# Kernel tuning notes

Hardware: AMD Instinct MI355X
Metric: run time of the kernel (lower is better)

## Reference

```python
import jax, jax.numpy as jnp
import numpy as np

B, N, DIM, HID, H, K, NNEG, MAXLEN, NUMALL = 4096, 50, 64, 64, 4, 10, 4, 512, 100000
NITEM = 50  # config onesample_size


def pe_table(max_len, dim):
    pos = jnp.arange(max_len, dtype=jnp.float32)[:, None]
    div = jnp.exp(jnp.arange(0, dim, 2, dtype=jnp.float32) * (-np.log(10000.0) / dim))
    ang = pos * div
    pe = jnp.zeros((max_len, dim), jnp.float32)
    return pe.at[:, 0::2].set(jnp.sin(ang)).at[:, 1::2].set(jnp.cos(ang))


def gat(x, adj, W_gat, a_src, a_dst, W_o):
    # x: (b,n,d), adj: (b,n,n) binary
    Wh = jnp.einsum('bnd,hdk->bhnk', x, W_gat)
    es = jnp.einsum('bhnk,hk->bhn', Wh, a_src)
    ed = jnp.einsum('bhnk,hk->bhn', Wh, a_dst)
    e = jax.nn.leaky_relu(es[:, :, :, None] + ed[:, :, None, :], 0.2)
    e = jnp.where(adj[:, None] > 0, e, -1e9)
    attn = jax.nn.softmax(e, axis=-1)
    out = jnp.einsum('bhnm,bhmk->bhnk', attn, Wh)
    out = out.transpose(0, 2, 1, 3).reshape(x.shape[0], x.shape[1], -1)
    return jax.nn.elu(out @ W_o)


def aggregate(x, cand):
    # attention-pool x (b,n,d) per candidate (b,c,d) -> (b,c,d)
    attn = jax.nn.softmax(jnp.einsum('bnd,bcd->bcn', x, cand), axis=-1)
    return jnp.einsum('bcn,bnd->bcd', attn, x)


def ssl_topk(user, pos, neg, tao=0.5):
    nrm = lambda v: v / jnp.linalg.norm(v, axis=-1, keepdims=True)
    user, pos, neg = nrm(user), nrm(pos), nrm(neg)
    ps = jnp.sum(jnp.exp(jnp.einsum('bkd,bd->bk', pos, user) / tao), axis=1)
    ns = jnp.sum(jnp.exp(jnp.einsum('bkd,bd->bk', neg, user) / tao), axis=1)
    return -jnp.mean(jnp.log(ps) - jnp.log(ps + ns))


def setup_inputs():
    key = jax.random.key(0)
    ks = jax.random.split(key, 14)
    d = {}
    d['emb_table'] = jax.random.normal(ks[0], (NUMALL + 1, DIM)) * 0.1
    d['W_PE'] = jax.random.normal(ks[1], (DIM, DIM)) * 0.1
    d['W_pred'] = jax.random.normal(ks[2], (2 * DIM, DIM)) * 0.1
    d['W_gat'] = jax.random.normal(ks[3], (H, DIM, HID)) * 0.1
    d['a_src'] = jax.random.normal(ks[4], (H, HID)) * 0.1
    d['a_dst'] = jax.random.normal(ks[5], (H, HID)) * 0.1
    d['W_o'] = jax.random.normal(ks[6], (H * HID, DIM)) * 0.1
    d['W_assign'] = jax.random.normal(ks[7], (DIM, K)) * 0.1
    d['adj'] = (jax.random.uniform(ks[8], (B, N, N)) > 0.5).astype(jnp.float32)
    d['history'] = jax.random.randint(ks[9], (B, N), 0, NUMALL)
    d['timestp'] = jax.random.randint(ks[10], (B, N), 0, MAXLEN)
    d['pos_id'] = jax.random.randint(ks[11], (B, 1), 0, NUMALL)
    d['neg_id'] = jax.random.randint(ks[12], (B, NNEG), 0, NUMALL)
    d['stp'] = jax.random.randint(ks[13], (B, 1), 0, MAXLEN)
    return d


def reference(emb_table, W_PE, W_pred, W_gat, a_src, a_dst, W_o, W_assign,
              adj, history, timestp, pos_id, neg_id, stp):
    pe = pe_table(MAXLEN, DIM)
    _x = emb_table[history]            # (B,N,D)
    pos = emb_table[pos_id]            # (B,1,D)
    neg = emb_table[neg_id]            # (B,NNEG,D)
    cand = jnp.concatenate([pos, neg], axis=1)  # (B,C,D)
    mask_base = (history > 0)[:, :, None].astype(_x.dtype)
    x = (_x + pe[timestp] @ W_PE) * mask_base
    cand = cand + pe[stp] @ W_PE       # broadcast PE over all candidates
    # ParentNodeLayer: soft assignment pooling (DiffPool-style)
    s = jax.nn.softmax(x @ W_assign, axis=-1)          # (B,N,K)
    x_parent = jnp.einsum('bnk,bnd->bkd', s, x)        # (B,K,D)
    # GAT over item sub-graph
    x_new_I = gat(x[:, :NITEM], adj[:, :NITEM, :NITEM], W_gat, a_src, a_dst, W_o)
    # candidate-conditioned aggregation + prediction (vectorized over candidates)
    u_F = aggregate(x_parent, cand)
    u_I = aggregate(x_new_I, cand)
    u = jnp.concatenate([u_F, u_I], axis=-1) @ W_pred  # (B,C,D)
    scores = jnp.sum(u * cand, axis=-1)                # (B,C)
    pos_s, neg_s = scores[:, :1], scores[:, 1:]
    loss = jnp.mean(jax.nn.softplus(neg_s - pos_s))
    s_m = s[:, :NITEM]
    loss_entropy = -jnp.sum(s_m * jnp.log(s_m)) / (NITEM * B)
    loss_reg = (jnp.sum(_x ** 2) + jnp.sum(pos ** 2) + jnp.sum(neg ** 2)) / float(B) \
               + jnp.sum(W_pred ** 2) + jnp.sum(W_PE ** 2)
    # contrastive branch (dropout in eval mode == identity)
    user_I = jnp.mean(x_new_I, axis=1)
    user_F = jnp.mean(x_parent, axis=1)
    sI = jnp.einsum('bcd,bd->bc', cand, user_I)
    sF = jnp.einsum('bcd,bd->bc', cand, user_F)
    n_cand = cand.shape[1]
    _, ind_I = jax.lax.top_k(sI, n_cand)
    _, ind_F = jax.lax.top_k(sF, n_cand)
    gather = lambda ind: jnp.take_along_axis(cand, ind[:, :, None], axis=1)
    C = 2
    loss_con = ssl_topk(user_I, gather(ind_F[:, :2]), gather(ind_F[:, 2:2 + C])) \
             + ssl_topk(user_F, gather(ind_I[:, :2]), gather(ind_I[:, 2:2 + C]))
    return jnp.stack([loss, loss_reg, loss_entropy, loss_con])
```

## Files before the change

kernel.cpp:

```cpp
#include <hip/hip_runtime.h>
#include <hip/hip_bf16.h>
#include <math.h>

typedef __hip_bfloat16 bf16;
typedef __attribute__((ext_vector_type(8))) short sv8;
typedef __attribute__((ext_vector_type(4))) short sv4;
typedef __attribute__((ext_vector_type(4))) float fv4;

__device__ __forceinline__ float b2f(bf16 v){ return __bfloat162float(v); }
__device__ __forceinline__ bf16  f2b(float v){ return __float2bfloat16(v); }
__device__ __forceinline__ short f2bs(float v){ bf16 h=__float2bfloat16(v); short s; __builtin_memcpy(&s,&h,2); return s; }
__device__ __forceinline__ float bs2f(short s){ bf16 h; __builtin_memcpy(&h,&s,2); return __bfloat162float(h); }
__device__ __forceinline__ fv4 MFMA(sv8 a, sv8 b, fv4 c){
  return __builtin_amdgcn_mfma_f32_16x16x32_bf16(a,b,c,0,0,0);
}
__device__ __forceinline__ int pk2(float a, float b){
  unsigned sa=(unsigned short)f2bs(a);
  unsigned sb=((unsigned)(unsigned short)f2bs(b))<<16;
  return (int)(sa|sb);
}
__device__ __forceinline__ int pk2s(short a, short b){
  return (int)(((unsigned short)a) | (((unsigned)(unsigned short)b)<<16));
}
union U8 { int i[4]; sv8 v; };

__global__ __launch_bounds__(64) void k_pe(const float* __restrict__ Wpe, float* __restrict__ pewt)
{
  const int t=blockIdx.x, d=threadIdx.x;
  __shared__ float pr[64];
  const float c0 = -logf(10000.f)/32.f;
  float ang = (float)t * expf((float)(d>>1)*c0);
  pr[d] = (d&1)? cosf(ang) : sinf(ang);
  __syncthreads();
  float a=0.f;
  #pragma unroll 8
  for(int j=0;j<64;j++) a += pr[j]*Wpe[j*64+d];
  pewt[t*64+d]=a;
}

__global__ __launch_bounds__(256) void k_prep(
    const float* __restrict__ Wg, const float* __restrict__ Wo,
    const float* __restrict__ as_, const float* __restrict__ ad_,
    const float* __restrict__ Wassign, const float* __restrict__ Wpred,
    short* __restrict__ wgb, short* __restrict__ wob, short* __restrict__ asb,
    short* __restrict__ wab, short* __restrict__ wpb)
{
  int i = blockIdx.x*256+threadIdx.x;
  {
    int j=i&7, lane=(i>>3)&63, ks=(i>>9)&1, nt=(i>>10)&3, h=(i>>12)&3;
    int c=lane&15, q=lane>>4;
    int k=ks*32+q*8+j;
    wgb[i] = f2bs(Wg[h*4096 + k*64 + nt*16 + c]);
    wob[i] = f2bs(Wo[(size_t)(h*64 + k)*64 + nt*16 + c]);
  }
  if(i<4096){
    int j=i&7, lane=(i>>3)&63, ks=(i>>9)&1, h=(i>>10)&3;
    int c=lane&15, q=lane>>4; int k=ks*32+q*8+j;
    float v = (c==0)? as_[h*64+k] : (c==1? ad_[h*64+k] : 0.f);
    asb[i]=f2bs(v);
  }
  if(i<1024){
    int j=i&7, lane=(i>>3)&63, ks=(i>>9)&1;
    int c=lane&15, q=lane>>4; int k=ks*32+q*8+j;
    wab[i] = (c<10)? f2bs(Wassign[k*10+c]) : (short)0;
  }
  if(i<8192){
    int j=i&7, lane=(i>>3)&63, ks=(i>>9)&3, nt=(i>>11)&3;
    int c=lane&15, q=lane>>4; int k=ks*32+q*8+j;
    wpb[i] = f2bs(Wpred[k*64 + nt*16 + c]);
  }
}

__global__ __launch_bounds__(256,4) void kmain(
    const float* __restrict__ emb, const float* __restrict__ pewt,
    const int* __restrict__ history, const int* __restrict__ timestp,
    const int* __restrict__ pos_id, const int* __restrict__ neg_id, const int* __restrict__ stp,
    const float* __restrict__ adj,
    const short* __restrict__ wgb, const short* __restrict__ wob, const short* __restrict__ asb,
    const short* __restrict__ wab, const short* __restrict__ wpb,
    float* __restrict__ reg_part, float* __restrict__ ent_part,
    float* __restrict__ loss_part, float* __restrict__ con_part)
{
  const int b=blockIdx.x, tid=threadIdx.x;
  const int h=tid>>6, lane=tid&63;
  const int c=lane&15, q=lane>>4;

  __shared__ __align__(16) char arena[36864];
  char*  PP    = arena + h*7200;
  short* xs_s  = (short*)(arena+14400);
  float* es_f  = (float*)(arena+28800 + h*768);
  float* ed_f  = es_f + 64;
  float* inv_f = es_f + 128;
  float* cndF  = (float*)(arena+31872);
  float* xplF  = (float*)(arena+33152);
  float* uFvec = (float*)(arena+35712);
  float* uacc  = (float*)(arena+35968);
  int*   hist  = (int*)(arena+36224);
  int*   tvals = (int*)(arena+36424);
  int*   ids   = (int*)(arena+36624);
  int*   stv   = (int*)(arena+36644);
  float* ph    = (float*)(arena+36648);
  float* scF   = (float*)(arena+36664);
  float* sIv   = scF+5;
  float* sFv   = scF+10;
  float* cnv   = scF+15;
  float* un    = scF+20;
  float* sbF   = (float*)arena;

  if (tid < 50) hist[tid] = history[b*50+tid];
  if (tid >= 64 && tid < 114) tvals[tid-64] = timestp[b*50+(tid-64)];
  if (tid == 128) stv[0] = stp[b];
  if (tid == 129) ids[0] = pos_id[b];
  if (tid >= 130 && tid < 134) ids[tid-129] = neg_id[b*4+(tid-130)];

  unsigned long long mymask=0ULL;
  {
    const float* adjb = adj + (size_t)b*2500;
    for(int n=0;n<50;n++){
      float av = (lane<50)? adjb[n*50+lane] : 0.f;
      unsigned long long mk = __ballot(av>0.f);
      if(lane==n) mymask = mk;
    }
  }
  __syncthreads();

  float regp=0.f;
  for (int i=tid;i<3200;i+=256){
    int n=i>>6, d=i&63;
    float ev=emb[(size_t)hist[n]*64 + d];
    regp += ev*ev;
    float v = (hist[n]>0) ? (ev + pewt[tvals[n]*64+d]) : 0.f;
    xs_s[n*72+d]=f2bs(v);
  }
  for (int i=tid;i<320;i+=256){
    int cc=i>>6, d=i&63;
    float ev=emb[(size_t)ids[cc]*64+d];
    regp += ev*ev;
    cndF[i]=ev + pewt[stv[0]*64+d];
  }
  #pragma unroll
  for(int m=1;m<64;m<<=1) regp += __shfl_xor(regp,m,64);
  if(lane==0) ph[h]=regp;
  __syncthreads();

  sv8 af[4][2];
  #pragma unroll
  for(int mt=0;mt<4;mt++){
    int r = mt*16 + c; if(r>=50) r=0;
    #pragma unroll
    for(int ks=0;ks<2;ks++)
      af[mt][ks] = *(const sv8*)(xs_s + r*72 + ks*32 + q*8);
  }
  {
    sv8 wa0 = *(const sv8*)(wab + (0*64+lane)*8);
    sv8 wa1 = *(const sv8*)(wab + (1*64+lane)*8);
    fv4 acc={0.f,0.f,0.f,0.f};
    acc = MFMA(af[h][0], wa0, acc);
    acc = MFMA(af[h][1], wa1, acc);
    #pragma unroll
    for(int reg=0;reg<4;reg++){
      int n=16*h+4*q+reg;
      if(n<50 && c<10) sbF[n*10+c]=acc[reg];
    }
  }
  __syncthreads();
  if(tid==0) reg_part[b]=ph[0]+ph[1]+ph[2]+ph[3];

  float entp=0.f;
  if (tid<50){
    float mx=-1e30f;
    for(int k=0;k<10;k++) mx=fmaxf(mx, sbF[tid*10+k]);
    float e[10], sm=0.f;
    for(int k=0;k<10;k++){ e[k]=expf(sbF[tid*10+k]-mx); sm+=e[k]; }
    float inv=1.f/sm;
    for(int k=0;k<10;k++){ float sv=e[k]*inv; sbF[tid*10+k]=sv; entp += sv*logf(sv); }
  }
  if(h==0){
    #pragma unroll
    for(int m=1;m<64;m<<=1) entp += __shfl_xor(entp,m,64);
    if(lane==0) ent_part[b]=entp;
  }
  __syncthreads();

  {
    sv8 sa[2], sxb[2];
    #pragma unroll
    for(int ks=0;ks<2;ks++){
      U8 ua, ub_;
      #pragma unroll
      for(int t2=0;t2<4;t2++){
        int n0=32*ks+8*q+2*t2, n1=n0+1;
        short lo=(n0<50 && c<10)? f2bs(sbF[n0*10+c]) : (short)0;
        short hi=(n1<50 && c<10)? f2bs(sbF[n1*10+c]) : (short)0;
        ua.i[t2]=pk2s(lo,hi);
        short lo2=(n0<50)? xs_s[n0*72+16*h+c] : (short)0;
        short hi2=(n1<50)? xs_s[n1*72+16*h+c] : (short)0;
        ub_.i[t2]=pk2s(lo2,hi2);
      }
      sa[ks]=ua.v; sxb[ks]=ub_.v;
    }
    fv4 acc={0.f,0.f,0.f,0.f};
    acc = MFMA(sa[0], sxb[0], acc);
    acc = MFMA(sa[1], sxb[1], acc);
    #pragma unroll
    for(int reg=0;reg<4;reg++){
      int k=4*q+reg;
      if(k<10) xplF[k*64+16*h+c]=acc[reg];
    }
  }
  __syncthreads();
  if(tid<64){
    float a=0.f;
    for(int k=0;k<10;k++) a += xplF[(k<<6)+tid];
    uFvec[tid]=a*0.1f;
  }

  int wh_pk[4][4][2];
  #pragma unroll
  for(int nt=0;nt<4;nt++){
    sv8 b0 = *(const sv8*)(wgb + (((h*4+nt)*2+0)*64 + lane)*8);
    sv8 b1 = *(const sv8*)(wgb + (((h*4+nt)*2+1)*64 + lane)*8);
    #pragma unroll
    for(int mt=0;mt<4;mt++){
      fv4 acc={0.f,0.f,0.f,0.f};
      acc = MFMA(af[mt][0], b0, acc);
      acc = MFMA(af[mt][1], b1, acc);
      wh_pk[mt][nt][0]=pk2(acc[0],acc[1]);
      wh_pk[mt][nt][1]=pk2(acc[2],acc[3]);
    }
  }
  {
    sv8 a5b0 = *(const sv8*)(asb + ((h*2+0)*64 + lane)*8);
    sv8 a5b1 = *(const sv8*)(asb + ((h*2+1)*64 + lane)*8);
    #pragma unroll
    for(int mt=0;mt<4;mt++){
      fv4 acc={0.f,0.f,0.f,0.f};
      acc = MFMA(af[mt][0], a5b0, acc);
      acc = MFMA(af[mt][1], a5b1, acc);
      if(c==0){
        #pragma unroll
        for(int reg=0;reg<4;reg++) es_f[mt*16+4*q+reg]=acc[reg];
      } else if(c==1){
        #pragma unroll
        for(int reg=0;reg<4;reg++) ed_f[mt*16+4*q+reg]=acc[reg];
      }
    }
  }
  {
    float es_n = es_f[lane];
    float sum=0.f;
    #pragma unroll
    for(int mb=0;mb<48;mb+=4){
      sv4 wv;
      #pragma unroll
      for(int jj=0;jj<4;jj++){
        int m=mb+jj;
        float z = es_n + ed_f[m];
        float lr = (z>0.f)? z : 0.2f*z;
        float p = ((mymask>>m)&1ULL)? expf(lr) : 0.f;
        wv[jj]=f2bs(p); sum+=p;
      }
      if(lane<50) *(sv4*)(PP + lane*144 + mb*2) = wv;
    }
    {
      sv4 wv={0,0,0,0};
      #pragma unroll
      for(int jj=0;jj<2;jj++){
        int m=48+jj;
        float z = es_n + ed_f[m];
        float lr = (z>0.f)? z : 0.2f*z;
        float p = ((mymask>>m)&1ULL)? expf(lr) : 0.f;
        wv[jj]=f2bs(p); sum+=p;
      }
      if(lane<50){
        *(sv4*)(PP + lane*144 + 48*2) = wv;
        sv4 zz={0,0,0,0};
        *(sv4*)(PP + lane*144 + 52*2) = zz;
        *(sv4*)(PP + lane*144 + 56*2) = zz;
        *(sv4*)(PP + lane*144 + 60*2) = zz;
      }
    }
    inv_f[lane] = (lane<50)? 1.f/sum : 0.f;
  }
  {
    sv8 ap[4][2];
    #pragma unroll
    for(int mt=0;mt<4;mt++){
      int r = mt*16+c; if(r>=50) r=0;
      #pragma unroll
      for(int ks=0;ks<2;ks++)
        ap[mt][ks] = *(const sv8*)(PP + r*144 + (ks*32+q*8)*2);
    }
    float invr[16];
    #pragma unroll
    for(int mt=0;mt<4;mt++)
      #pragma unroll
      for(int reg=0;reg<4;reg++) invr[mt*4+reg]=inv_f[mt*16+4*q+reg];

    const int L = c + ((q&1)<<5);
    const bool hi = (q>>1)!=0;
    #pragma unroll
    for(int nt=0;nt<4;nt++){
      sv8 bfr[2];
      #pragma unroll
      for(int ks=0;ks<2;ks++){
        int a0=__shfl(wh_pk[2*ks+0][nt][0],L,64), b0=__shfl(wh_pk[2*ks+1][nt][0],L,64);
        int a1=__shfl(wh_pk[2*ks+0][nt][1],L,64), b1=__shfl(wh_pk[2*ks+1][nt][1],L,64);
        int a2=__shfl(wh_pk[2*ks+0][nt][0],L+16,64), b2=__shfl(wh_pk[2*ks+1][nt][0],L+16,64);
        int a3=__shfl(wh_pk[2*ks+0][nt][1],L+16,64), b3=__shfl(wh_pk[2*ks+1][nt][1],L+16,64);
        U8 u;
        u.i[0]=hi?b0:a0; u.i[1]=hi?b1:a1; u.i[2]=hi?b2:a2; u.i[3]=hi?b3:a3;
        bfr[ks]=u.v;
      }
      #pragma unroll
      for(int mt=0;mt<4;mt++){
        fv4 acc={0.f,0.f,0.f,0.f};
        acc = MFMA(ap[mt][0], bfr[0], acc);
        acc = MFMA(ap[mt][1], bfr[1], acc);
        #pragma unroll
        for(int reg=0;reg<4;reg++){
          int row=mt*16+4*q+reg;
          if(row<50)
            *(short*)(PP + row*144 + (nt*16+c)*2) = f2bs(acc[reg]*invr[mt*4+reg]);
        }
      }
    }
  }
  {
    sv8 ao[4][2];
    #pragma unroll
    for(int mt=0;mt<4;mt++){
      int r = mt*16+c; if(r>=50) r=0;
      #pragma unroll
      for(int ks=0;ks<2;ks++)
        ao[mt][ks] = *(const sv8*)(PP + r*144 + (ks*32+q*8)*2);
    }
    #pragma unroll
    for(int nt=0;nt<4;nt++){
      sv8 bfr[2];
      #pragma unroll
      for(int ks=0;ks<2;ks++)
        bfr[ks] = *(const sv8*)(wob + (((h*4+nt)*2+ks)*64 + lane)*8);
      #pragma unroll
      for(int mt=0;mt<4;mt++){
        fv4 acc={0.f,0.f,0.f,0.f};
        acc = MFMA(ao[mt][0], bfr[0], acc);
        acc = MFMA(ao[mt][1], bfr[1], acc);
        #pragma unroll
        for(int reg=0;reg<4;reg++){
          int row=mt*16+4*q+reg;
          if(row<50)
            *(short*)(PP + row*144 + (nt*16+c)*2) = f2bs(acc[reg]);
        }
      }
    }
  }
  __syncthreads();

  float ve[13];
  {
    int ii=0;
    for(int i=tid;i<3200;i+=256,ii++){
      int n=i>>6, d=i&63;
      float v=0.f;
      #pragma unroll
      for(int hh=0;hh<4;hh++)
        v += bs2f(*(const short*)(arena + hh*7200 + n*144 + d*2));
      v = (v>0.f)? v : expm1f(v);
      ve[ii]=v;
    }
  }
  __syncthreads();

  float* xnl =(float*)arena;
  float* lF  =(float*)(arena+12800);
  float* lI  =(float*)(arena+13000);
  short* ubA =(short*)(arena+14400);
  short* xnlb=(short*)(arena+18752);

  {
    int ii=0;
    for(int i=tid;i<3200;i+=256,ii++){
      int n=i>>6, d=i&63;
      xnl[i]=ve[ii];
      xnlb[n*72+d]=f2bs(ve[ii]);
    }
  }
  __syncthreads();

  if(tid<64){
    float a=0.f;
    #pragma unroll 10
    for(int n=0;n<50;n++) a += xnl[(n<<6)+tid];
    uacc[tid]=a*0.02f;
  }
  for(int idx=h; idx<50; idx+=4){
    int k=idx%10, cc=idx/10;
    float s = xplF[(k<<6)+lane]*cndF[(cc<<6)+lane];
    #pragma unroll
    for(int m=32;m>0;m>>=1) s += __shfl_xor(s,m,64);
    if(lane==0) lF[idx]=s;
  }
  {
    sv8 al[2], bl[2];
    int r = 16*h + c; if(r>=50) r=0;
    #pragma unroll
    for(int ks=0;ks<2;ks++){
      al[ks] = *(const sv8*)(xnlb + r*72 + ks*32 + q*8);
      U8 u;
      #pragma unroll
      for(int t2=0;t2<4;t2++){
        int k0=ks*32+q*8+2*t2, k1=k0+1;
        short lo=(c<5)? f2bs(cndF[c*64+k0]) : (short)0;
        short hi=(c<5)? f2bs(cndF[c*64+k1]) : (short)0;
        u.i[t2]=pk2s(lo,hi);
      }
      bl[ks]=u.v;
    }
    fv4 acc={0.f,0.f,0.f,0.f};
    acc = MFMA(al[0], bl[0], acc);
    acc = MFMA(al[1], bl[1], acc);
    #pragma unroll
    for(int reg=0;reg<4;reg++){
      int row=16*h+4*q+reg;
      if(row<50 && c<5) lI[c*50+row]=acc[reg];
    }
  }
  __syncthreads();

  for(int cc=h; cc<5; cc+=4){
    float v = (lane<50)? lI[cc*50+lane] : -1e30f;
    float mx=v;
    #pragma unroll
    for(int m=32;m>0;m>>=1) mx=fmaxf(mx,__shfl_xor(mx,m,64));
    float e=(lane<50)? expf(v-mx):0.f;
    float sm=e;
    #pragma unroll
    for(int m=32;m>0;m>>=1) sm+=__shfl_xor(sm,m,64);
    if(lane<50) lI[cc*50+lane]=e/sm;
    float v2=(lane<10)? lF[cc*10+lane] : -1e30f;
    float mx2=v2;
    #pragma unroll
    for(int m=32;m>0;m>>=1) mx2=fmaxf(mx2,__shfl_xor(mx2,m,64));
    float e2=(lane<10)? expf(v2-mx2):0.f;
    float sm2=e2;
    #pragma unroll
    for(int m=32;m>0;m>>=1) sm2+=__shfl_xor(sm2,m,64);
    if(lane<10) lF[cc*10+lane]=e2/sm2;
  }
  __syncthreads();

  for(int i=tid;i<320;i+=256){
    int cc=i>>6, d=i&63;
    float a=0.f;
    for(int k=0;k<10;k++) a += lF[cc*10+k]*xplF[(k<<6)+d];
    float a2=0.f;
    for(int n2=0;n2<50;n2++) a2 += lI[cc*50+n2]*xnl[(n2<<6)+d];
    ubA[cc*136+d]=f2bs(a);
    ubA[cc*136+64+d]=f2bs(a2);
  }
  for(int i=tid;i<1496;i+=256){
    int row=5+i/136, col=i-136*(i/136);
    ubA[row*136+col]=0;
  }
  __syncthreads();

  if(h==0){
    sv8 ua[4];
    #pragma unroll
    for(int ks=0;ks<4;ks++)
      ua[ks] = *(const sv8*)(ubA + c*136 + ks*32 + q*8);
    float pr[4]={0.f,0.f,0.f,0.f};
    #pragma unroll
    for(int nt=0;nt<4;nt++){
      fv4 acc={0.f,0.f,0.f,0.f};
      #pragma unroll
      for(int ks=0;ks<4;ks++)
        acc = MFMA(ua[ks], *(const sv8*)(wpb + ((nt*4+ks)*64+lane)*8), acc);
      #pragma unroll
      for(int reg=0;reg<4;reg++){
        int cc=4*q+reg;
        if(cc<5) pr[reg] += acc[reg]*cndF[cc*64+16*nt+c];
      }
    }
    #pragma unroll
    for(int reg=0;reg<4;reg++){
      #pragma unroll
      for(int m=1;m<16;m<<=1) pr[reg]+=__shfl_xor(pr[reg],m,64);
    }
    if(c==0){
      #pragma unroll
      for(int reg=0;reg<4;reg++){
        int cc=4*q+reg;
        if(cc<5) scF[cc]=pr[reg];
      }
    }
  } else {
    for(int idx=4+h; idx<22; idx+=3){
      float va, vb;
      if(idx<10){ int cc=idx-5; va=cndF[(cc<<6)+lane]; vb=uacc[lane]; }
      else if(idx<15){ int cc=idx-10; va=cndF[(cc<<6)+lane]; vb=uFvec[lane]; }
      else if(idx<20){ int cc=idx-15; va=cndF[(cc<<6)+lane]; vb=va; }
      else if(idx==20){ va=uacc[lane]; vb=va; }
      else { va=uFvec[lane]; vb=va; }
      float s=va*vb;
      #pragma unroll
      for(int m=32;m>0;m>>=1) s += __shfl_xor(s,m,64);
      if(lane==0){
        if(idx<10) sIv[idx-5]=s;
        else if(idx<15) sFv[idx-10]=s;
        else if(idx<20) cnv[idx-15]=sqrtf(s);
        else un[idx-20]=sqrtf(s);
      }
    }
  }
  __syncthreads();

  if(tid==0){
    float lp=0.f;
    for(int cc=1;cc<5;cc++){
      float z=scF[cc]-scF[0];
      lp += fmaxf(z,0.f)+log1pf(expf(-fabsf(z)));
    }
    int indF[5], indI[5];
    { bool used[5]={0,0,0,0,0};
      for(int p=0;p<5;p++){ int best=0; float bv=-3e38f;
        for(int cc=0;cc<5;cc++) if(!used[cc]&&sFv[cc]>bv){bv=sFv[cc];best=cc;}
        used[best]=true; indF[p]=best; } }
    { bool used[5]={0,0,0,0,0};
      for(int p=0;p<5;p++){ int best=0; float bv=-3e38f;
        for(int cc=0;cc<5;cc++) if(!used[cc]&&sIv[cc]>bv){bv=sIv[cc];best=cc;}
        used[best]=true; indI[p]=best; } }
    float t1,t2;
    {
      float inv=2.f/un[0];
      float ps=expf(sIv[indF[0]]/cnv[indF[0]]*inv)+expf(sIv[indF[1]]/cnv[indF[1]]*inv);
      float ns=expf(sIv[indF[2]]/cnv[indF[2]]*inv)+expf(sIv[indF[3]]/cnv[indF[3]]*inv);
      t1=log1pf(ns/ps);
    }
    {
      float inv=2.f/un[1];
      float ps=expf(sFv[indI[0]]/cnv[indI[0]]*inv)+expf(sFv[indI[1]]/cnv[indI[1]]*inv);
      float ns=expf(sFv[indI[2]]/cnv[indI[2]]*inv)+expf(sFv[indI[3]]/cnv[indI[3]]*inv);
      t2=log1pf(ns/ps);
    }
    loss_part[b]=lp;
    con_part[b]=t1+t2;
  }
}

__global__ __launch_bounds__(256) void k3(
    const float* __restrict__ Wpred, const float* __restrict__ Wpe,
    const float* __restrict__ reg_part, const float* __restrict__ ent_part,
    const float* __restrict__ loss_part, const float* __restrict__ con_part,
    float* __restrict__ out)
{
  const int tid=threadIdx.x, h=tid>>6, lane=tid&63;
  __shared__ float r5[5][4];
  float s[5]={0.f,0.f,0.f,0.f,0.f};
  for(int i=tid;i<4096;i+=256){
    s[0]+=reg_part[i]; s[1]+=ent_part[i]; s[2]+=loss_part[i]; s[3]+=con_part[i];
  }
  for(int i=tid;i<8192;i+=256){ float w=Wpred[i]; s[4]+=w*w; }
  for(int i=tid;i<4096;i+=256){ float w=Wpe[i]; s[4]+=w*w; }
  #pragma unroll
  for(int t2=0;t2<5;t2++){
    float v=s[t2];
    #pragma unroll
    for(int m=1;m<64;m<<=1) v+=__shfl_xor(v,m,64);
    if(lane==0) r5[t2][h]=v;
  }
  __syncthreads();
  if(tid==0){
    float tot[5];
    for(int t2=0;t2<5;t2++) tot[t2]=r5[t2][0]+r5[t2][1]+r5[t2][2]+r5[t2][3];
    out[0]=tot[2]/(4096.f*4.f);
    out[1]=tot[0]/4096.f + tot[4];
    out[2]=-tot[1]/(50.f*4096.f);
    out[3]=tot[3]/4096.f;
  }
}

extern "C" void kernel_launch(void* const* d_in, const int* in_sizes, int n_in,
                              void* d_out, int out_size, void* d_ws, size_t ws_size,
                              hipStream_t stream)
{
  const float* emb     =(const float*)d_in[0];
  const float* Wpe     =(const float*)d_in[1];
  const float* Wpred   =(const float*)d_in[2];
  const float* Wgat    =(const float*)d_in[3];
  const float* a_src   =(const float*)d_in[4];
  const float* a_dst   =(const float*)d_in[5];
  const float* Wo      =(const float*)d_in[6];
  const float* Wassign =(const float*)d_in[7];
  const float* adj     =(const float*)d_in[8];
  const int* history  =(const int*)d_in[9];
  const int* timestp  =(const int*)d_in[10];
  const int* pos_id   =(const int*)d_in[11];
  const int* neg_id   =(const int*)d_in[12];
  const int* stp      =(const int*)d_in[13];
  float* out=(float*)d_out;

  char* ws=(char*)d_ws;
  float* reg_part =(float*)(ws+0);
  float* ent_part =(float*)(ws+16384);
  float* loss_part=(float*)(ws+32768);
  float* con_part =(float*)(ws+49152);
  float* pewt     =(float*)(ws+65536);
  short* wgb      =(short*)(ws+196608);
  short* wob      =(short*)(ws+229376);
  short* asb      =(short*)(ws+262144);
  short* wab      =(short*)(ws+270336);
  short* wpb      =(short*)(ws+272384);

  k_pe<<<512,64,0,stream>>>(Wpe,pewt);
  k_prep<<<64,256,0,stream>>>(Wgat,Wo,a_src,a_dst,Wassign,Wpred,wgb,wob,asb,wab,wpb);
  kmain<<<4096,256,0,stream>>>(emb,pewt,history,timestp,pos_id,neg_id,stp,adj,
                               wgb,wob,asb,wab,wpb,reg_part,ent_part,loss_part,con_part);
  k3<<<1,256,0,stream>>>(Wpred,Wpe,reg_part,ent_part,loss_part,con_part,out);
}
```

Before: 486.6 us.

## Merge PE and weight-prep kernels; compute Wh tiles just-in-time to cut registers

Combines the positional-encoding kernel and the weight-packing kernel into a single launch, with block ranges split between the two jobs, which removes one kernel launch. In the main kernel, the per-head Wh projection is no longer computed up front and kept live in 32 packed registers across the attention section. Each nt tile is now computed right before it is shuffled into the attention-times-Wh MFMA, which shortens register live ranges and may raise occupancy or avoid spills. The cost is that the wgb weight loads and the Wh MFMAs are moved into the later loop.

```diff
diff --git a/kernel.cpp b/kernel.cpp
--- a/kernel.cpp
+++ b/kernel.cpp
@@ -24,50 +24,51 @@
 }
 union U8 { int i[4]; sv8 v; };
 
-__global__ __launch_bounds__(64) void k_pe(const float* __restrict__ Wpe, float* __restrict__ pewt)
-{
-  const int t=blockIdx.x, d=threadIdx.x;
-  __shared__ float pr[64];
-  const float c0 = -logf(10000.f)/32.f;
-  float ang = (float)t * expf((float)(d>>1)*c0);
-  pr[d] = (d&1)? cosf(ang) : sinf(ang);
-  __syncthreads();
-  float a=0.f;
-  #pragma unroll 8
-  for(int j=0;j<64;j++) a += pr[j]*Wpe[j*64+d];
-  pewt[t*64+d]=a;
-}
-
-__global__ __launch_bounds__(256) void k_prep(
-    const float* __restrict__ Wg, const float* __restrict__ Wo,
+__global__ __launch_bounds__(256) void k_pre(
+    const float* __restrict__ Wpe, const float* __restrict__ Wg, const float* __restrict__ Wo,
     const float* __restrict__ as_, const float* __restrict__ ad_,
     const float* __restrict__ Wassign, const float* __restrict__ Wpred,
-    short* __restrict__ wgb, short* __restrict__ wob, short* __restrict__ asb,
-    short* __restrict__ wab, short* __restrict__ wpb)
+    float* __restrict__ pewt, short* __restrict__ wgb, short* __restrict__ wob,
+    short* __restrict__ asb, short* __restrict__ wab, short* __restrict__ wpb)
 {
-  int i = blockIdx.x*256+threadIdx.x;
-  {
-    int j=i&7, lane=(i>>3)&63, ks=(i>>9)&1, nt=(i>>10)&3, h=(i>>12)&3;
-    int c=lane&15, q=lane>>4;
-    int k=ks*32+q*8+j;
-    wgb[i] = f2bs(Wg[h*4096 + k*64 + nt*16 + c]);
-    wob[i] = f2bs(Wo[(size_t)(h*64 + k)*64 + nt*16 + c]);
-  }
-  if(i<4096){
-    int j=i&7, lane=(i>>3)&63, ks=(i>>9)&1, h=(i>>10)&3;
-    int c=lane&15, q=lane>>4; int k=ks*32+q*8+j;
-    float v = (c==0)? as_[h*64+k] : (c==1? ad_[h*64+k] : 0.f);
-    asb[i]=f2bs(v);
-  }
-  if(i<1024){
-    int j=i&7, lane=(i>>3)&63, ks=(i>>9)&1;
-    int c=lane&15, q=lane>>4; int k=ks*32+q*8+j;
-    wab[i] = (c<10)? f2bs(Wassign[k*10+c]) : (short)0;
-  }
-  if(i<8192){
-    int j=i&7, lane=(i>>3)&63, ks=(i>>9)&3, nt=(i>>11)&3;
-    int c=lane&15, q=lane>>4; int k=ks*32+q*8+j;
-    wpb[i] = f2bs(Wpred[k*64 + nt*16 + c]);
+  const int blk=blockIdx.x, tid=threadIdx.x;
+  if(blk<128){
+    __shared__ float pr[4][64];
+    int w=tid>>6, d=tid&63;
+    int t=blk*4+w;
+    const float c0 = -logf(10000.f)/32.f;
+    float ang=(float)t*expf((float)(d>>1)*c0);
+    pr[w][d]=(d&1)? cosf(ang) : sinf(ang);
+    __syncthreads();
+    float a=0.f;
+    #pragma unroll 8
+    for(int j=0;j<64;j++) a += pr[w][j]*Wpe[j*64+d];
+    pewt[t*64+d]=a;
+  } else {
+    int i=(blk-128)*256+tid;
+    {
+      int j=i&7, lane=(i>>3)&63, ks=(i>>9)&1, nt=(i>>10)&3, h=(i>>12)&3;
+      int c=lane&15, q=lane>>4;
+      int k=ks*32+q*8+j;
+      wgb[i] = f2bs(Wg[h*4096 + k*64 + nt*16 + c]);
+      wob[i] = f2bs(Wo[(size_t)(h*64 + k)*64 + nt*16 + c]);
+    }
+    if(i<4096){
+      int j=i&7, lane=(i>>3)&63, ks=(i>>9)&1, h=(i>>10)&3;
+      int c=lane&15, q=lane>>4; int k=ks*32+q*8+j;
+      float v = (c==0)? as_[h*64+k] : (c==1? ad_[h*64+k] : 0.f);
+      asb[i]=f2bs(v);
+    }
+    if(i<1024){
+      int j=i&7, lane=(i>>3)&63, ks=(i>>9)&1;
+      int c=lane&15, q=lane>>4; int k=ks*32+q*8+j;
+      wab[i] = (c<10)? f2bs(Wassign[k*10+c]) : (short)0;
+    }
+    if(i<8192){
+      int j=i&7, lane=(i>>3)&63, ks=(i>>9)&3, nt=(i>>11)&3;
+      int c=lane&15, q=lane>>4; int k=ks*32+q*8+j;
+      wpb[i] = f2bs(Wpred[k*64 + nt*16 + c]);
+    }
   }
 }
 
@@ -215,20 +216,6 @@
     uFvec[tid]=a*0.1f;
   }
 
-  int wh_pk[4][4][2];
-  #pragma unroll
-  for(int nt=0;nt<4;nt++){
-    sv8 b0 = *(const sv8*)(wgb + (((h*4+nt)*2+0)*64 + lane)*8);
-    sv8 b1 = *(const sv8*)(wgb + (((h*4+nt)*2+1)*64 + lane)*8);
-    #pragma unroll
-    for(int mt=0;mt<4;mt++){
-      fv4 acc={0.f,0.f,0.f,0.f};
-      acc = MFMA(af[mt][0], b0, acc);
-      acc = MFMA(af[mt][1], b1, acc);
-      wh_pk[mt][nt][0]=pk2(acc[0],acc[1]);
-      wh_pk[mt][nt][1]=pk2(acc[2],acc[3]);
-    }
-  }
   {
     sv8 a5b0 = *(const sv8*)(asb + ((h*2+0)*64 + lane)*8);
     sv8 a5b1 = *(const sv8*)(asb + ((h*2+1)*64 + lane)*8);
@@ -301,13 +288,26 @@
     const bool hi = (q>>1)!=0;
     #pragma unroll
     for(int nt=0;nt<4;nt++){
+      int wt[4][2];
+      {
+        sv8 b0 = *(const sv8*)(wgb + (((h*4+nt)*2+0)*64 + lane)*8);
+        sv8 b1 = *(const sv8*)(wgb + (((h*4+nt)*2+1)*64 + lane)*8);
+        #pragma unroll
+        for(int mt=0;mt<4;mt++){
+          fv4 acc={0.f,0.f,0.f,0.f};
+          acc = MFMA(af[mt][0], b0, acc);
+          acc = MFMA(af[mt][1], b1, acc);
+          wt[mt][0]=pk2(acc[0],acc[1]);
+          wt[mt][1]=pk2(acc[2],acc[3]);
+        }
+      }
       sv8 bfr[2];
       #pragma unroll
       for(int ks=0;ks<2;ks++){
-        int a0=__shfl(wh_pk[2*ks+0][nt][0],L,64), b0=__shfl(wh_pk[2*ks+1][nt][0],L,64);
-        int a1=__shfl(wh_pk[2*ks+0][nt][1],L,64), b1=__shfl(wh_pk[2*ks+1][nt][1],L,64);
-        int a2=__shfl(wh_pk[2*ks+0][nt][0],L+16,64), b2=__shfl(wh_pk[2*ks+1][nt][0],L+16,64);
-        int a3=__shfl(wh_pk[2*ks+0][nt][1],L+16,64), b3=__shfl(wh_pk[2*ks+1][nt][1],L+16,64);
+        int a0=__shfl(wt[2*ks+0][0],L,64), b0=__shfl(wt[2*ks+1][0],L,64);
+        int a1=__shfl(wt[2*ks+0][1],L,64), b1=__shfl(wt[2*ks+1][1],L,64);
+        int a2=__shfl(wt[2*ks+0][0],L+16,64), b2=__shfl(wt[2*ks+1][0],L+16,64);
+        int a3=__shfl(wt[2*ks+0][1],L+16,64), b3=__shfl(wt[2*ks+1][1],L+16,64);
         U8 u;
         u.i[0]=hi?b0:a0; u.i[1]=hi?b1:a1; u.i[2]=hi?b2:a2; u.i[3]=hi?b3:a3;
         bfr[ks]=u.v;
@@ -613,8 +613,8 @@
   short* wab      =(short*)(ws+270336);
   short* wpb      =(short*)(ws+272384);
 
-  k_pe<<<512,64,0,stream>>>(Wpe,pewt);
-  k_prep<<<64,256,0,stream>>>(Wgat,Wo,a_src,a_dst,Wassign,Wpred,wgb,wob,asb,wab,wpb);
+  k_pre<<<192,256,0,stream>>>(Wpe,Wgat,Wo,a_src,a_dst,Wassign,Wpred,
+                              pewt,wgb,wob,asb,wab,wpb);
   kmain<<<4096,256,0,stream>>>(emb,pewt,history,timestp,pos_id,neg_id,stp,adj,
                                wgb,wob,asb,wab,wpb,reg_part,ent_part,loss_part,con_part);
   k3<<<1,256,0,stream>>>(Wpred,Wpe,reg_part,ent_part,loss_part,con_part,out);
```

Result: faster. 437.0 us (-10.2%).
